# Kernel optimization log

Measured on AMD Instinct MI355X. Metric: run time of the kernel, lower is better.

## Reference

```python
import jax, jax.numpy as jnp
import numpy as np

LSTM = 256
NUM_CELLS = 5
BLOCKS = 6
TEMP = 5.0
TANH_C = 1.1


def setup_inputs() -> dict:
    key = jax.random.key(0)
    ks = jax.random.split(key, 8)
    s = 0.05  # small init so sigmoids/tanh stay in sane range
    return {
        "enc_w": jax.random.normal(ks[0], (5, LSTM), jnp.float32) * s,
        "w_ih": jax.random.normal(ks[1], (4 * LSTM, LSTM), jnp.float32) * s,
        "w_hh": jax.random.normal(ks[2], (4 * LSTM, LSTM), jnp.float32) * s,
        "b_ih": jax.random.normal(ks[3], (4 * LSTM,), jnp.float32) * s,
        "b_hh": jax.random.normal(ks[4], (4 * LSTM,), jnp.float32) * s,
        "w1": jax.random.normal(ks[5], (LSTM, LSTM), jnp.float32) * s,
        "w2": jax.random.normal(ks[6], (LSTM, LSTM), jnp.float32) * s,
        "v": jax.random.normal(ks[7], (LSTM,), jnp.float32) * s,
    }


def _lstm_cell(x, h, c, w_ih, w_hh, b_ih, b_hh):
    # torch.nn.LSTMCell gate order: i, f, g, o
    g = w_ih @ x + b_ih + w_hh @ h + b_hh  # [4*LSTM]
    i, f, gg, o = jnp.split(g, 4)
    i, f, o = jax.nn.sigmoid(i), jax.nn.sigmoid(f), jax.nn.sigmoid(o)
    c2 = f * c + i * jnp.tanh(gg)
    h2 = o * jnp.tanh(c2)
    return h2, c2


def _run_sampler(bkey, enc_w, w_ih, w_hh, b_ih, b_hh, w1, w2, v):
    zeros = jnp.zeros((LSTM,), jnp.float32)
    inputs = enc_w[0]  # encoder(0)
    anchors = []
    anchors_w1 = []
    prev_h = prev_c = zeros
    # first two layers: LSTM always fed zero state (faithful to source)
    for _ in range(2):
        prev_h, prev_c = _lstm_cell(inputs, zeros, zeros, w_ih, w_hh, b_ih, b_hh)
        anchors.append(zeros)
        anchors_w1.append(w1 @ prev_h)
    arc_seq, log_probs, entropies = [], [], []
    step = 0
    for layer_id in range(2, NUM_CELLS + 2):
        for _ in range(2):
            prev_h, prev_c = _lstm_cell(inputs, prev_h, prev_c, w_ih, w_hh, b_ih, b_hh)
            q = jnp.tanh(jnp.stack(anchors_w1[:layer_id]) + w2 @ prev_h)  # [layer_id, LSTM]
            logits = (q @ v) / TEMP  # [layer_id]
            logits = TANH_C * jnp.tanh(logits)
            skey = jax.random.fold_in(bkey, step); step += 1
            index = jax.random.categorical(skey, logits)
            lsm = jax.nn.log_softmax(logits)
            arc_seq.append(index)
            log_probs.append(-lsm[index])  # F.cross_entropy
            entropies.append(jax.lax.stop_gradient(-jnp.sum(lsm * jnp.exp(lsm))))
            inputs = jnp.stack(anchors[:layer_id])[index]
        prev_h, prev_c = _lstm_cell(inputs, prev_h, prev_c, w_ih, w_hh, b_ih, b_hh)
        anchors.append(prev_h)
        anchors_w1.append(w1 @ prev_h)
        inputs = enc_w[0]
    arc = jnp.stack(arc_seq)  # [2*NUM_CELLS] int
    return arc, sum(entropies), sum(log_probs), prev_c, prev_h


def reference(enc_w, w_ih, w_hh, b_ih, b_hh, w1, w2, v):
    key = jax.random.key(42)
    all_arc = []
    all_entropy = jnp.float32(0.0)
    all_log_prob = jnp.float32(0.0)
    c = h = None
    for b in range(BLOCKS):
        arc, ent, lp, c, h = _run_sampler(
            jax.random.fold_in(key, b), enc_w, w_ih, w_hh, b_ih, b_hh, w1, w2, v)
        all_arc.append(arc)
        all_entropy = all_entropy + ent
        all_log_prob = all_log_prob + lp
    return (jnp.stack(all_arc), all_log_prob, all_entropy, c[None, :], h[None, :])
```

## Files before the change

kernel.cpp:

```cpp
#include <hip/hip_runtime.h>
#include <stdint.h>


#define NBLK  6
#define PWG   8
#define THR   512
#define TINYF 1.17549435e-38f
#define HTAGB 0xC3B00000u
#define YTAGB 0xE1700000u
#define ITAGB 0xA5D00000u
#define DONE_MAGIC 0x444f4e45

typedef unsigned long long u64;
struct U2 { uint32_t x, y; };

#define W_DONE 0u
#define W_PART 64u
#define W_IDX  128u
#define W_HX   640u
#define W_YMB  25216u
#define W_NEED 126976u

#define S_READY 0u
#define S_DONE  192u
#define S_PART  224u
#define S_HP    320u
#define S_ACC   24896u
#define FXS     67108864.0f
#define READY_MAGIC 0x52454459

__device__ __forceinline__ U2 tf2x32(uint32_t k0, uint32_t k1,
                                     uint32_t c0, uint32_t c1) {
  uint32_t ks2 = k0 ^ k1 ^ 0x1BD11BDAu;
  uint32_t x0 = c0 + k0, x1 = c1 + k1;
#define TFR(r) { x0 += x1; x1 = (x1 << (r)) | (x1 >> (32 - (r))); x1 ^= x0; }
  TFR(13) TFR(15) TFR(26) TFR(6)   x0 += k1;  x1 += ks2 + 1u;
  TFR(17) TFR(29) TFR(16) TFR(24)  x0 += ks2; x1 += k0 + 2u;
  TFR(13) TFR(15) TFR(26) TFR(6)   x0 += k0;  x1 += k1 + 3u;
  TFR(17) TFR(29) TFR(16) TFR(24)  x0 += k1;  x1 += ks2 + 4u;
  TFR(13) TFR(15) TFR(26) TFR(6)   x0 += ks2; x1 += k0 + 5u;
#undef TFR
  U2 r; r.x = x0; r.y = x1; return r;
}

__device__ __forceinline__ float sigf(float x) {
  return 1.0f / (1.0f + expf(-x));
}
__device__ __forceinline__ void istore(int* p, int v) {
  __hip_atomic_store(p, v, __ATOMIC_RELAXED, __HIP_MEMORY_SCOPE_AGENT);
}
__device__ __forceinline__ int iload(const int* p) {
  return __hip_atomic_load(p, __ATOMIC_RELAXED, __HIP_MEMORY_SCOPE_AGENT);
}
__device__ __forceinline__ void hstore(u64* p, u64 v) {
  __hip_atomic_store(p, v, __ATOMIC_RELAXED, __HIP_MEMORY_SCOPE_AGENT);
}
__device__ __forceinline__ u64 hload(const u64* p) {
  return __hip_atomic_load(p, __ATOMIC_RELAXED, __HIP_MEMORY_SCOPE_AGENT);
}
__device__ __forceinline__ void fstore(float* p, float v) {
  __hip_atomic_store(p, v, __ATOMIC_RELAXED, __HIP_MEMORY_SCOPE_AGENT);
}
__device__ __forceinline__ float fload(const float* p) {
  return __hip_atomic_load(p, __ATOMIC_RELAXED, __HIP_MEMORY_SCOPE_AGENT);
}
__device__ __forceinline__ u64 pollw(const u64* p, uint32_t want) {
  u64 v;
  for (;;) {
    v = hload(p);
    if ((uint32_t)(v >> 32) == want) return v;
    __builtin_amdgcn_s_sleep(1);
  }
}

__global__ __launch_bounds__(THR, 2) void ctrl_v11(
    const float* __restrict__ enc_w,
    const float* __restrict__ wih,
    const float* __restrict__ whh,
    const float* __restrict__ b_ih,
    const float* __restrict__ b_hh,
    const float* __restrict__ w1,
    const float* __restrict__ w2,
    const float* __restrict__ vvec,
    unsigned char* __restrict__ ws,
    float* __restrict__ out) {

  const int b = blockIdx.x & 7;
  const int p = blockIdx.x >> 3;
  if (b >= NBLK) return;
  const int tid = threadIdx.x;

  int*   done = (int*)(ws + W_DONE);
  float* part = (float*)(ws + W_PART);
  u64*   idxw = (u64*)(ws + W_IDX);
  u64*   hx   = (u64*)(ws + W_HX);
  u64*   ymb  = (u64*)(ws + W_YMB);

  const int rl = tid & 127, s = tid >> 7;
  const int grow = (rl >> 5) * 256 + p * 32 + (rl & 31);
  const int k0 = s * 64;
  const int rr = tid & 255, ks = tid >> 8;
  const int cb = p * 32 + ks * 16;

  __shared__ __align__(16) float gateL[THR];
  __shared__ __align__(16) float hL[256], encL[256], vL[256];
  __shared__ __align__(16) float anchL[4][256];
  __shared__ __align__(16) float w2hS[256], aw1S[6][256];
  __shared__ __align__(16) float yL8[8][256];
  __shared__ float rowSumL[128], biasS[128], h2S[32];
  __shared__ float logitL[8];
  __shared__ int   selL;

  if (tid < 256) { encL[tid] = enc_w[tid]; vL[tid] = vvec[tid]; }
  if (tid < 128) {
    int r = (tid >> 5) * 256 + p * 32 + (tid & 31);
    biasS[tid] = b_ih[r] + b_hh[r];
  }

  float4 wihr[16], whhr[16];
  #pragma unroll
  for (int c = 0; c < 16; ++c) {
    wihr[c] = *(const float4*)(wih + grow * 256 + k0 + c * 4);
    whhr[c] = *(const float4*)(whh + grow * 256 + k0 + c * 4);
  }
  float w1c[16], w2c[16];
  #pragma unroll
  for (int j = 0; j < 16; ++j) {
    w1c[j] = w1[rr * 256 + cb + j];
    w2c[j] = w2[rr * 256 + cb + j];
  }
  __syncthreads();

  auto dotIH = [&](const float* x) {
    float a = 0.0f;
    #pragma unroll
    for (int c = 0; c < 16; ++c) {
      float4 xv = *(const float4*)(x + k0 + c * 4);
      float4 w = wihr[c];
      a += w.x * xv.x + w.y * xv.y + w.z * xv.z + w.w * xv.w;
    }
    return a;
  };
  auto dotHH = [&]() {
    float a = 0.0f;
    #pragma unroll
    for (int c = 0; c < 16; ++c) {
      float4 xv = *(const float4*)(hL + k0 + c * 4);
      float4 w = whhr[c];
      a += w.x * xv.x + w.y * xv.y + w.z * xv.z + w.w * xv.w;
    }
    return a;
  };

  const float encih = dotIH(encL);

  float cv = 0.0f;
  U2 bk = tf2x32(0u, 42u, 0u, (uint32_t)b);
  int k = 1, step = 0;
  float lpAcc = 0.0f, entAcc = 0.0f;

  auto cell = [&](float gacc, int mode, int aid, int cid) {
    gateL[tid] = gacc;
    __syncthreads();
    if (tid < 128) {
      float ssum = 0.0f;
      #pragma unroll
      for (int j = 0; j < 4; ++j) ssum += gateL[j * 128 + tid];
      rowSumL[tid] = ssum + biasS[tid];
    }
    __syncthreads();
    if (tid < 32) {
      float gi = rowSumL[tid],       gf = rowSumL[32 + tid];
      float gg2 = rowSumL[64 + tid], go = rowSumL[96 + tid];
      float c2 = sigf(gf) * cv + sigf(gi) * tanhf(gg2);
      float h2 = sigf(go) * tanhf(c2);
      cv = c2;
      h2S[tid] = h2;
      if (mode == 2) {
        if (b == NBLK - 1) { out[62 + p * 32 + tid] = cv; out[318 + p * 32 + tid] = h2; }
      } else {
        hstore(&hx[(k & 1) * 1536 + b * 256 + p * 32 + tid],
               ((u64)(HTAGB | (uint32_t)k) << 32) | (u64)__float_as_uint(h2));
      }
    }
    __syncthreads();
    if (mode == 2) return;

    {
      const float* wc = (mode == 1) ? w1c : w2c;
      float yp = 0.0f;
      #pragma unroll
      for (int j = 0; j < 16; ++j) yp += wc[j] * h2S[ks * 16 + j];
      gateL[tid] = yp;
    }
    __syncthreads();
    u64* mslot = ymb + (size_t)(k & 1) * 6192 + (b * 8 + p) * 129;
    if (tid < 128) {
      float ya = gateL[2 * tid]     + gateL[256 + 2 * tid];
      float yb = gateL[2 * tid + 1] + gateL[256 + 2 * tid + 1];
      hstore(mslot + tid,
             ((u64)__float_as_uint(yb) << 32) | (u64)__float_as_uint(ya));
    }
    __syncthreads();
    if (tid == 0)
      hstore(mslot + 128, ((u64)(YTAGB | (uint32_t)k) << 32) | 1u);

    if (tid < 256) {
      u64 v = pollw(&hx[(k & 1) * 1536 + b * 256 + tid], HTAGB | (uint32_t)k);
      float hv = __uint_as_float((uint32_t)v);
      hL[tid] = hv;
      if (mode == 1 && cid >= 0) anchL[cid][tid] = hv;
    }
    __syncthreads();

    if (p == 0) {
      if (tid < 8)
        pollw(ymb + (size_t)(k & 1) * 6192 + (b * 8 + tid) * 129 + 128,
              YTAGB | (uint32_t)k);
      __syncthreads();
      {
        int pw = tid >> 6, o = tid & 63;
        const u64* mb = ymb + (size_t)(k & 1) * 6192 + (b * 8 + pw) * 129;
        u64 wa = hload(mb + 2 * o), wb = hload(mb + 2 * o + 1);
        yL8[pw][4 * o + 0] = __uint_as_float((uint32_t)wa);
        yL8[pw][4 * o + 1] = __uint_as_float((uint32_t)(wa >> 32));
        yL8[pw][4 * o + 2] = __uint_as_float((uint32_t)wb);
        yL8[pw][4 * o + 3] = __uint_as_float((uint32_t)(wb >> 32));
      }
      __syncthreads();
      if (tid < 256) {
        float y = 0.0f;
        #pragma unroll
        for (int pw = 0; pw < 8; ++pw) y += yL8[pw][tid];
        if (mode == 1) aw1S[aid][tid] = y; else w2hS[tid] = y;
      }
      __syncthreads();
    }
    ++k;
  };

  auto resolve = [&](int L) -> int {
    if (p == 0) {
      int wv = tid >> 6, lane = tid & 63;
      if (wv < L) {
        float a = 0.0f;
        #pragma unroll
        for (int j = 0; j < 4; ++j) {
          int kk = j * 64 + lane;
          a += tanhf(aw1S[wv][kk] + w2hS[kk]) * vL[kk];
        }
        a += __shfl_down(a, 32);
        a += __shfl_down(a, 16);
        a += __shfl_down(a, 8);
        a += __shfl_down(a, 4);
        a += __shfl_down(a, 2);
        a += __shfl_down(a, 1);
        if (lane == 0) logitL[wv] = a;
      }
      __syncthreads();
      if (tid < 64) {
        float lg = 0.0f, sgum = -1e30f;
        if (tid < L) {
          lg = 1.1f * tanhf(logitL[tid] * 0.2f);
          U2 sk = tf2x32(bk.x, bk.y, 0u, (uint32_t)step);
          U2 r2 = tf2x32(sk.x, sk.y, 0u, (uint32_t)tid);
          uint32_t bits = r2.x ^ r2.y;
          float u = __uint_as_float((bits >> 9) | 0x3f800000u) - 1.0f;
          u = fmaxf(TINYF, u + TINYF);
          sgum = lg - logf(-logf(u));
        }
        int bi = 0;
        float best = __shfl(sgum, 0, 64);
        for (int j = 1; j < L; ++j) {
          float sj = __shfl(sgum, j, 64);
          if (sj > best) { best = sj; bi = j; }
        }
        float mx = __shfl(lg, 0, 64);
        for (int j = 1; j < L; ++j) mx = fmaxf(mx, __shfl(lg, j, 64));
        float se = 0.0f;
        for (int j = 0; j < L; ++j) se += expf(__shfl(lg, j, 64) - mx);
        float lse = logf(se);
        float lgbi = __shfl(lg, bi, 64);
        float es = 0.0f;
        for (int j = 0; j < L; ++j) {
          float l = __shfl(lg, j, 64) - mx - lse;
          es += l * expf(l);
        }
        if (tid == 0) {
          lpAcc += -(lgbi - mx - lse);
          entAcc += -es;
          selL = bi;
          out[b * 10 + step] = (float)bi;
          hstore(&idxw[b * 10 + step],
                 ((u64)(ITAGB | (uint32_t)step) << 32) | (u64)(uint32_t)bi);
        }
      }
      __syncthreads();
    } else {
      if (tid == 0) {
        u64 v = pollw(&idxw[b * 10 + step], ITAGB | (uint32_t)step);
        selL = (int)(uint32_t)v;
      }
      __syncthreads();
    }
    step++;
    return selL;
  };

  cell(encih, 1, 0, -1);
  if (p == 0) {
    if (tid < 256) aw1S[1][tid] = aw1S[0][tid];
    __syncthreads();
  }

  for (int L = 2; L <= 6; ++L) {
    { float hh = dotHH(); cell(encih + hh, 0, 0, -1); }
    {
      int s1; float hh;
      if (p == 0) { s1 = resolve(L); hh = dotHH(); }
      else        { hh = dotHH(); s1 = resolve(L); }
      float a = (s1 >= 2) ? dotIH(&anchL[s1 - 2][0]) : 0.0f;
      cell(a + hh, 0, 0, -1);
    }
    {
      int s2; float hh;
      if (p == 0) { s2 = resolve(L); hh = dotHH(); }
      else        { hh = dotHH(); s2 = resolve(L); }
      float a = (s2 >= 2) ? dotIH(&anchL[s2 - 2][0]) : 0.0f;
      if (L < 6) cell(a + hh, 1, L, L - 2);
      else       cell(a + hh, 2, 0, -1);
    }
  }

  if (p == 0 && tid == 0) {
    fstore(&part[2 * b], lpAcc);
    fstore(&part[2 * b + 1], entAcc);
    __builtin_amdgcn_s_waitcnt(0);
    istore(&done[b], DONE_MAGIC);
    if (b == NBLK - 1) {
      float lp = 0.0f, en = 0.0f;
      for (int j = 0; j < NBLK; ++j) {
        while (iload(&done[j]) != DONE_MAGIC) __builtin_amdgcn_s_sleep(1);
        lp += fload(&part[2 * j]);
        en += fload(&part[2 * j + 1]);
      }
      out[60] = lp;
      out[61] = en;
    }
  }
}

__global__ __launch_bounds__(1024) void ctrl_small(
    const float* __restrict__ enc_w,
    const float* __restrict__ wih,
    const float* __restrict__ whh,
    const float* __restrict__ b_ih,
    const float* __restrict__ b_hh,
    const float* __restrict__ w1,
    const float* __restrict__ w2,
    const float* __restrict__ vvec,
    unsigned char* __restrict__ ws,
    float* __restrict__ out) {

  const int b = blockIdx.x & 7;
  const int p = blockIdx.x >> 3;
  if (b >= NBLK) return;
  const int tid = threadIdx.x;

  int*   ready = (int*)(ws + S_READY);
  int*   done  = (int*)(ws + S_DONE);
  float* part  = (float*)(ws + S_PART);
  u64*   hp    = (u64*)(ws + S_HP);
  int*   acc   = (int*)(ws + S_ACC);

  const int rl = tid >> 3, s = tid & 7;
  const int g = rl >> 5, el = rl & 31;
  const int row = g * 256 + p * 32 + el;
  const int k0 = s * 32;
  const int rr = tid & 255, ks = tid >> 8;

  __shared__ __align__(16) float hL[256], encL[256], vL[256];
  __shared__ __align__(16) float anchL[4][256];
  __shared__ __align__(16) float partL[1024];
  __shared__ __align__(16) float w2hS[256], aw1S[6][256];
  __shared__ float rowSumL[128], biasS[128], h2S[32];
  __shared__ float logitL[8];
  __shared__ int   selL;

  if (tid < 256) { encL[tid] = enc_w[tid]; vL[tid] = vvec[tid]; }
  if (tid < 128) {
    int gg = tid >> 5, ee = tid & 31, r = gg * 256 + p * 32 + ee;
    biasS[tid] = b_ih[r] + b_hh[r];
  }

  float4 wihr[8], whhr[8];
  #pragma unroll
  for (int c = 0; c < 8; ++c) {
    int cc = (c + s) & 7;
    wihr[c] = *(const float4*)(wih + row * 256 + k0 + cc * 4);
    whhr[c] = *(const float4*)(whh + row * 256 + k0 + cc * 4);
  }
  float w1c[8], w2c[8];
  #pragma unroll
  for (int j = 0; j < 8; ++j) {
    w1c[j] = w1[rr * 256 + p * 32 + ks * 8 + j];
    w2c[j] = w2[rr * 256 + p * 32 + ks * 8 + j];
  }

  if (tid < 32) istore(&acc[1 * (NBLK * 256) + b * 256 + p * 32 + tid], 0);
  __syncthreads();
  if (tid == 0) istore(&ready[b * 8 + p], READY_MAGIC);
  if (tid < 8) {
    while (iload(&ready[b * 8 + tid]) != READY_MAGIC)
      __builtin_amdgcn_s_sleep(1);
  }
  __syncthreads();

  auto dotIH = [&](const float* x) {
    float a = 0.0f;
    #pragma unroll
    for (int c = 0; c < 8; ++c) {
      int cc = (c + s) & 7;
      float4 xv = *(const float4*)(x + k0 + cc * 4);
      float4 w = wihr[c];
      a += w.x * xv.x + w.y * xv.y + w.z * xv.z + w.w * xv.w;
    }
    return a;
  };
  auto dotHH = [&]() {
    float a = 0.0f;
    #pragma unroll
    for (int c = 0; c < 8; ++c) {
      int cc = (c + s) & 7;
      float4 xv = *(const float4*)(hL + k0 + cc * 4);
      float4 w = whhr[c];
      a += w.x * xv.x + w.y * xv.y + w.z * xv.z + w.w * xv.w;
    }
    return a;
  };

  const float encih = dotIH(encL);
  float cv = 0.0f;
  U2 bk = tf2x32(0u, 42u, 0u, (uint32_t)b);
  int k = 1, step = 0;
  float lpAcc = 0.0f, entAcc = 0.0f;

  auto cell = [&](float gacc, int mode, int aid, int cid) {
    partL[tid] = gacc;
    __syncthreads();
    if (tid < 128) {
      float ssum = 0.0f;
      #pragma unroll
      for (int j = 0; j < 8; ++j) ssum += partL[tid * 8 + j];
      rowSumL[tid] = ssum + biasS[tid];
    }
    __syncthreads();
    if (tid < 32) {
      float gi = rowSumL[tid],       gf = rowSumL[32 + tid];
      float gg2 = rowSumL[64 + tid], go = rowSumL[96 + tid];
      float c2 = sigf(gf) * cv + sigf(gi) * tanhf(gg2);
      float h2 = sigf(go) * tanhf(c2);
      cv = c2;
      h2S[tid] = h2;
      if (mode == 2 && b == NBLK - 1) {
        out[62 + p * 32 + tid] = cv;
        out[318 + p * 32 + tid] = h2;
      }
    }
    __syncthreads();
    if (mode == 2) return;
    {
      const float* wc = (mode == 1) ? w1c : w2c;
      float yp = 0.0f;
      #pragma unroll
      for (int j = 0; j < 8; ++j) yp += wc[j] * h2S[ks * 8 + j];
      atomicAdd(&acc[(k % 3) * (NBLK * 256) + b * 256 + rr],
                __float2int_rn(yp * FXS));
      if (tid < 32)
        istore(&acc[((k + 1) % 3) * (NBLK * 256) + b * 256 + p * 32 + tid], 0);
    }
    __syncthreads();
    if (tid < 32) {
      u64 pk = ((u64)(uint32_t)k << 32) | (u64)__float_as_uint(h2S[tid]);
      hstore(&hp[(k & 1) * (NBLK * 256) + b * 256 + p * 32 + tid], pk);
    }
    if (tid < 256) {
      u64 v;
      const u64* src = &hp[(k & 1) * (NBLK * 256) + b * 256 + tid];
      while ((int)(hload(src) >> 32) != k) __builtin_amdgcn_s_sleep(1);
      v = hload(src);
      float hv = __uint_as_float((uint32_t)v);
      hL[tid] = hv;
      if (mode == 1 && cid >= 0) anchL[cid][tid] = hv;
    }
    __syncthreads();
    if (tid < 256) {
      int iv = iload(&acc[(k % 3) * (NBLK * 256) + b * 256 + tid]);
      float f = (float)((double)iv * (1.0 / 67108864.0));
      if (mode == 1) aw1S[aid][tid] = f; else w2hS[tid] = f;
    }
    __syncthreads();
    ++k;
  };

  auto sample = [&](int L) -> int {
    int wv = tid >> 6, lane = tid & 63;
    if (wv < L) {
      float a = 0.0f;
      #pragma unroll
      for (int j = 0; j < 4; ++j) {
        int kk = lane * 4 + j;
        a += tanhf(aw1S[wv][kk] + w2hS[kk]) * vL[kk];
      }
      a += __shfl_down(a, 32);
      a += __shfl_down(a, 16);
      a += __shfl_down(a, 8);
      a += __shfl_down(a, 4);
      a += __shfl_down(a, 2);
      a += __shfl_down(a, 1);
      if (lane == 0) logitL[wv] = a;
    }
    __syncthreads();
    if (tid < 64) {
      float lg = 0.0f, sgum = -1e30f;
      if (tid < L) {
        lg = 1.1f * tanhf(logitL[tid] * 0.2f);
        U2 sk = tf2x32(bk.x, bk.y, 0u, (uint32_t)step);
        U2 r2 = tf2x32(sk.x, sk.y, 0u, (uint32_t)tid);
        uint32_t bits = r2.x ^ r2.y;
        float u = __uint_as_float((bits >> 9) | 0x3f800000u) - 1.0f;
        u = fmaxf(TINYF, u + TINYF);
        sgum = lg - logf(-logf(u));
      }
      int bi = 0;
      float best = __shfl(sgum, 0, 64);
      for (int j = 1; j < L; ++j) {
        float sj = __shfl(sgum, j, 64);
        if (sj > best) { best = sj; bi = j; }
      }
      float mx = __shfl(lg, 0, 64);
      for (int j = 1; j < L; ++j) mx = fmaxf(mx, __shfl(lg, j, 64));
      float se = 0.0f;
      for (int j = 0; j < L; ++j) se += expf(__shfl(lg, j, 64) - mx);
      float lse = logf(se);
      float lgbi = __shfl(lg, bi, 64);
      float es = 0.0f;
      for (int j = 0; j < L; ++j) {
        float l = __shfl(lg, j, 64) - mx - lse;
        es += l * expf(l);
      }
      if (tid == 0) {
        lpAcc += -(lgbi - mx - lse);
        entAcc += -es;
        selL = bi;
        if (p == 0) out[b * 10 + step] = (float)bi;
      }
    }
    __syncthreads();
    step++;
    return selL;
  };

  cell(encih, 1, 0, -1);
  if (tid < 256) aw1S[1][tid] = aw1S[0][tid];
  __syncthreads();
  for (int L = 2; L <= 6; ++L) {
    cell(encih + dotHH(), 0, 0, -1);
    int s1v = sample(L);
    {
      float a = (s1v >= 2) ? dotIH(&anchL[s1v - 2][0]) : 0.0f;
      cell(a + dotHH(), 0, 0, -1);
    }
    int s2v = sample(L);
    {
      float a = (s2v >= 2) ? dotIH(&anchL[s2v - 2][0]) : 0.0f;
      if (L < 6) cell(a + dotHH(), 1, L, L - 2);
      else       cell(a + dotHH(), 2, 0, -1);
    }
  }
  if (p == 0 && tid == 0) {
    fstore(&part[2 * b], lpAcc);
    fstore(&part[2 * b + 1], entAcc);
    __builtin_amdgcn_s_waitcnt(0);
    istore(&done[b], DONE_MAGIC);
    if (b == NBLK - 1) {
      float lp = 0.0f, en = 0.0f;
      for (int j = 0; j < NBLK; ++j) {
        while (iload(&done[j]) != DONE_MAGIC) __builtin_amdgcn_s_sleep(1);
        lp += fload(&part[2 * j]);
        en += fload(&part[2 * j + 1]);
      }
      out[60] = lp;
      out[61] = en;
    }
  }
}

extern "C" void kernel_launch(void* const* d_in, const int* in_sizes, int n_in,
                              void* d_out, int out_size, void* d_ws, size_t ws_size,
                              hipStream_t stream) {
  const float* enc = (const float*)d_in[0];
  const float* wih = (const float*)d_in[1];
  const float* whh = (const float*)d_in[2];
  const float* bih = (const float*)d_in[3];
  const float* bhh = (const float*)d_in[4];
  const float* w1  = (const float*)d_in[5];
  const float* w2  = (const float*)d_in[6];
  const float* v   = (const float*)d_in[7];
  unsigned char* ws = (unsigned char*)d_ws;
  float* out = (float*)d_out;

  if (ws_size >= W_NEED) {
    ctrl_v11<<<dim3(64), dim3(THR), 0, stream>>>(
        enc, wih, whh, bih, bhh, w1, w2, v, ws, out);
  } else {
    ctrl_small<<<dim3(64), dim3(1024), 0, stream>>>(
        enc, wih, whh, bih, bhh, w1, w2, v, ws, out);
  }
}
```

Measured before the change: 152.4 us.

## Replicate sampling on every workgroup and precompute anchor input projections

Every workgroup in a batch now reads the partial W1/W2 projections itself and runs the categorical sampling redundantly, with the same RNG. This removes the index broadcast from workgroup 0 and the extra poll round-trip that came with it. The input-weight dot product for each anchor is computed once, when the anchor is created, and kept in shared memory (aihS), so a later selection is just a lookup. W_ih is no longer held in registers, which lowers register pressure. The cost is duplicated reduction and sampling work in every workgroup, more global reads of the exchange buffers, and a hand-unrolled, fairly convoluted loop control flow.

```diff
diff --git a/kernel.cpp b/kernel.cpp
--- a/kernel.cpp
+++ b/kernel.cpp
@@ -8,7 +8,6 @@
 #define TINYF 1.17549435e-38f
 #define HTAGB 0xC3B00000u
 #define YTAGB 0xE1700000u
-#define ITAGB 0xA5D00000u
 #define DONE_MAGIC 0x444f4e45
 
 typedef unsigned long long u64;
@@ -16,10 +15,9 @@
 
 #define W_DONE 0u
 #define W_PART 64u
-#define W_IDX  128u
-#define W_HX   640u
-#define W_YMB  25216u
-#define W_NEED 126976u
+#define W_EX   512u
+#define EXBLK  161
+#define W_NEED 124160u
 
 #define S_READY 0u
 #define S_DONE  192u
@@ -73,7 +71,7 @@
   }
 }
 
-__global__ __launch_bounds__(THR, 2) void ctrl_v11(
+__global__ __launch_bounds__(THR, 2) void ctrl_v12(
     const float* __restrict__ enc_w,
     const float* __restrict__ wih,
     const float* __restrict__ whh,
@@ -92,9 +90,7 @@
 
   int*   done = (int*)(ws + W_DONE);
   float* part = (float*)(ws + W_PART);
-  u64*   idxw = (u64*)(ws + W_IDX);
-  u64*   hx   = (u64*)(ws + W_HX);
-  u64*   ymb  = (u64*)(ws + W_YMB);
+  u64*   ex   = (u64*)(ws + W_EX);
 
   const int rl = tid & 127, s = tid >> 7;
   const int grow = (rl >> 5) * 256 + p * 32 + (rl & 31);
@@ -104,12 +100,11 @@
 
   __shared__ __align__(16) float gateL[THR];
   __shared__ __align__(16) float hL[256], encL[256], vL[256];
-  __shared__ __align__(16) float anchL[4][256];
   __shared__ __align__(16) float w2hS[256], aw1S[6][256];
   __shared__ __align__(16) float yL8[8][256];
+  __shared__ __align__(16) float aihS[4][128];
   __shared__ float rowSumL[128], biasS[128], h2S[32];
   __shared__ float logitL[8];
-  __shared__ int   selL;
 
   if (tid < 256) { encL[tid] = enc_w[tid]; vL[tid] = vvec[tid]; }
   if (tid < 128) {
@@ -117,12 +112,10 @@
     biasS[tid] = b_ih[r] + b_hh[r];
   }
 
-  float4 wihr[16], whhr[16];
+  float4 whhr[16];
   #pragma unroll
-  for (int c = 0; c < 16; ++c) {
-    wihr[c] = *(const float4*)(wih + grow * 256 + k0 + c * 4);
+  for (int c = 0; c < 16; ++c)
     whhr[c] = *(const float4*)(whh + grow * 256 + k0 + c * 4);
-  }
   float w1c[16], w2c[16];
   #pragma unroll
   for (int j = 0; j < 16; ++j) {
@@ -131,16 +124,6 @@
   }
   __syncthreads();
 
-  auto dotIH = [&](const float* x) {
-    float a = 0.0f;
-    #pragma unroll
-    for (int c = 0; c < 16; ++c) {
-      float4 xv = *(const float4*)(x + k0 + c * 4);
-      float4 w = wihr[c];
-      a += w.x * xv.x + w.y * xv.y + w.z * xv.z + w.w * xv.w;
-    }
-    return a;
-  };
   auto dotHH = [&]() {
     float a = 0.0f;
     #pragma unroll
@@ -151,15 +134,26 @@
     }
     return a;
   };
-
-  const float encih = dotIH(encL);
+  auto dotIHg = [&](const float* x) {
+    const float4* wp = (const float4*)(wih + grow * 256 + k0);
+    float a = 0.0f;
+    #pragma unroll
+    for (int c = 0; c < 16; ++c) {
+      float4 w = wp[c];
+      float4 xv = *(const float4*)(x + k0 + c * 4);
+      a += w.x * xv.x + w.y * xv.y + w.z * xv.z + w.w * xv.w;
+    }
+    return a;
+  };
+
+  const float encih = dotIHg(encL);
 
   float cv = 0.0f;
   U2 bk = tf2x32(0u, 42u, 0u, (uint32_t)b);
-  int k = 1, step = 0;
+  int k = 1, kc = 0, step = 0;
   float lpAcc = 0.0f, entAcc = 0.0f;
 
-  auto cell = [&](float gacc, int mode, int aid, int cid) {
+  auto cell = [&](float gacc, bool isW1, bool last) {
     gateL[tid] = gacc;
     __syncthreads();
     if (tid < 128) {
@@ -169,6 +163,7 @@
       rowSumL[tid] = ssum + biasS[tid];
     }
     __syncthreads();
+    u64* blk = ex + (((size_t)(k & 1) * NBLK + b) * PWG + p) * EXBLK;
     if (tid < 32) {
       float gi = rowSumL[tid],       gf = rowSumL[32 + tid];
       float gg2 = rowSumL[64 + tid], go = rowSumL[96 + tid];
@@ -176,159 +171,205 @@
       float h2 = sigf(go) * tanhf(c2);
       cv = c2;
       h2S[tid] = h2;
-      if (mode == 2) {
+      if (last) {
         if (b == NBLK - 1) { out[62 + p * 32 + tid] = cv; out[318 + p * 32 + tid] = h2; }
       } else {
-        hstore(&hx[(k & 1) * 1536 + b * 256 + p * 32 + tid],
+        hstore(blk + 128 + tid,
                ((u64)(HTAGB | (uint32_t)k) << 32) | (u64)__float_as_uint(h2));
       }
     }
     __syncthreads();
-    if (mode == 2) return;
-
-    {
-      const float* wc = (mode == 1) ? w1c : w2c;
+    if (last) return;
+
+    {
+      const float* wc = isW1 ? w1c : w2c;
       float yp = 0.0f;
       #pragma unroll
       for (int j = 0; j < 16; ++j) yp += wc[j] * h2S[ks * 16 + j];
       gateL[tid] = yp;
     }
     __syncthreads();
-    u64* mslot = ymb + (size_t)(k & 1) * 6192 + (b * 8 + p) * 129;
     if (tid < 128) {
       float ya = gateL[2 * tid]     + gateL[256 + 2 * tid];
       float yb = gateL[2 * tid + 1] + gateL[256 + 2 * tid + 1];
-      hstore(mslot + tid,
+      hstore(blk + tid,
              ((u64)__float_as_uint(yb) << 32) | (u64)__float_as_uint(ya));
     }
     __syncthreads();
     if (tid == 0)
-      hstore(mslot + 128, ((u64)(YTAGB | (uint32_t)k) << 32) | 1u);
+      hstore(blk + 160, ((u64)(YTAGB | (uint32_t)k) << 32) | 1u);
 
     if (tid < 256) {
-      u64 v = pollw(&hx[(k & 1) * 1536 + b * 256 + tid], HTAGB | (uint32_t)k);
-      float hv = __uint_as_float((uint32_t)v);
-      hL[tid] = hv;
-      if (mode == 1 && cid >= 0) anchL[cid][tid] = hv;
-    }
-    __syncthreads();
-
-    if (p == 0) {
-      if (tid < 8)
-        pollw(ymb + (size_t)(k & 1) * 6192 + (b * 8 + tid) * 129 + 128,
-              YTAGB | (uint32_t)k);
-      __syncthreads();
-      {
-        int pw = tid >> 6, o = tid & 63;
-        const u64* mb = ymb + (size_t)(k & 1) * 6192 + (b * 8 + pw) * 129;
-        u64 wa = hload(mb + 2 * o), wb = hload(mb + 2 * o + 1);
-        yL8[pw][4 * o + 0] = __uint_as_float((uint32_t)wa);
-        yL8[pw][4 * o + 1] = __uint_as_float((uint32_t)(wa >> 32));
-        yL8[pw][4 * o + 2] = __uint_as_float((uint32_t)wb);
-        yL8[pw][4 * o + 3] = __uint_as_float((uint32_t)(wb >> 32));
-      }
-      __syncthreads();
-      if (tid < 256) {
-        float y = 0.0f;
-        #pragma unroll
-        for (int pw = 0; pw < 8; ++pw) y += yL8[pw][tid];
-        if (mode == 1) aw1S[aid][tid] = y; else w2hS[tid] = y;
-      }
-      __syncthreads();
-    }
+      const u64* base = ex + (((size_t)(k & 1) * NBLK + b) * PWG) * EXBLK;
+      u64 v = pollw(base + (size_t)(tid >> 5) * EXBLK + 128 + (tid & 31),
+                    HTAGB | (uint32_t)k);
+      hL[tid] = __uint_as_float((uint32_t)v);
+    }
+    __syncthreads();
+    kc = k;
     ++k;
   };
 
-  auto resolve = [&](int L) -> int {
-    if (p == 0) {
-      int wv = tid >> 6, lane = tid & 63;
-      if (wv < L) {
-        float a = 0.0f;
-        #pragma unroll
-        for (int j = 0; j < 4; ++j) {
-          int kk = j * 64 + lane;
-          a += tanhf(aw1S[wv][kk] + w2hS[kk]) * vL[kk];
-        }
-        a += __shfl_down(a, 32);
-        a += __shfl_down(a, 16);
-        a += __shfl_down(a, 8);
-        a += __shfl_down(a, 4);
-        a += __shfl_down(a, 2);
-        a += __shfl_down(a, 1);
-        if (lane == 0) logitL[wv] = a;
-      }
-      __syncthreads();
-      if (tid < 64) {
-        float lg = 0.0f, sgum = -1e30f;
-        if (tid < L) {
-          lg = 1.1f * tanhf(logitL[tid] * 0.2f);
-          U2 sk = tf2x32(bk.x, bk.y, 0u, (uint32_t)step);
-          U2 r2 = tf2x32(sk.x, sk.y, 0u, (uint32_t)tid);
-          uint32_t bits = r2.x ^ r2.y;
-          float u = __uint_as_float((bits >> 9) | 0x3f800000u) - 1.0f;
-          u = fmaxf(TINYF, u + TINYF);
-          sgum = lg - logf(-logf(u));
-        }
-        int bi = 0;
-        float best = __shfl(sgum, 0, 64);
-        for (int j = 1; j < L; ++j) {
-          float sj = __shfl(sgum, j, 64);
-          if (sj > best) { best = sj; bi = j; }
-        }
-        float mx = __shfl(lg, 0, 64);
-        for (int j = 1; j < L; ++j) mx = fmaxf(mx, __shfl(lg, j, 64));
+  auto finishY = [&](int aid, bool isW1) {
+    const u64* base = ex + (((size_t)(kc & 1) * NBLK + b) * PWG) * EXBLK;
+    if (tid < 8) pollw(base + (size_t)tid * EXBLK + 160, YTAGB | (uint32_t)kc);
+    __syncthreads();
+    {
+      int q = tid >> 6, w0 = (tid & 63) * 2;
+      const u64* mb = base + (size_t)q * EXBLK;
+      u64 wa = hload(mb + w0), wb = hload(mb + w0 + 1);
+      yL8[q][2 * w0 + 0] = __uint_as_float((uint32_t)wa);
+      yL8[q][2 * w0 + 1] = __uint_as_float((uint32_t)(wa >> 32));
+      yL8[q][2 * w0 + 2] = __uint_as_float((uint32_t)wb);
+      yL8[q][2 * w0 + 3] = __uint_as_float((uint32_t)(wb >> 32));
+    }
+    __syncthreads();
+    if (tid < 256) {
+      float y = 0.0f;
+      #pragma unroll
+      for (int q = 0; q < 8; ++q) y += yL8[q][tid];
+      if (isW1) aw1S[aid][tid] = y; else w2hS[tid] = y;
+    }
+    __syncthreads();
+  };
+
+  auto makeAih = [&](int cid) {
+    float a = dotIHg(hL);
+    gateL[tid] = a;
+    __syncthreads();
+    if (tid < 128) {
+      float ssum = 0.0f;
+      #pragma unroll
+      for (int j = 0; j < 4; ++j) ssum += gateL[j * 128 + tid];
+      aihS[cid][tid] = ssum;
+    }
+    __syncthreads();
+  };
+
+  auto sample = [&](int L) -> int {
+    int wv = tid >> 6, lane = tid & 63;
+    if (wv < L) {
+      float a = 0.0f;
+      #pragma unroll
+      for (int j = 0; j < 4; ++j) {
+        int kk = j * 64 + lane;
+        a += tanhf(aw1S[wv][kk] + w2hS[kk]) * vL[kk];
+      }
+      a += __shfl_down(a, 32);
+      a += __shfl_down(a, 16);
+      a += __shfl_down(a, 8);
+      a += __shfl_down(a, 4);
+      a += __shfl_down(a, 2);
+      a += __shfl_down(a, 1);
+      if (lane == 0) logitL[wv] = a;
+    }
+    __syncthreads();
+    int bi = 0;
+    {
+      float lg[6];
+      for (int i = 0; i < L; ++i) lg[i] = 1.1f * tanhf(logitL[i] * 0.2f);
+      U2 sk = tf2x32(bk.x, bk.y, 0u, (uint32_t)step);
+      float best = 0.0f;
+      for (int i = 0; i < L; ++i) {
+        U2 r2 = tf2x32(sk.x, sk.y, 0u, (uint32_t)i);
+        uint32_t bits = r2.x ^ r2.y;
+        float u = __uint_as_float((bits >> 9) | 0x3f800000u) - 1.0f;
+        u = fmaxf(TINYF, u + TINYF);
+        float sg = lg[i] - logf(-logf(u));
+        if (i == 0 || sg > best) { best = sg; bi = i; }
+      }
+      if (tid == 0) {
+        float mx = lg[0];
+        for (int i = 1; i < L; ++i) mx = fmaxf(mx, lg[i]);
         float se = 0.0f;
-        for (int j = 0; j < L; ++j) se += expf(__shfl(lg, j, 64) - mx);
+        for (int i = 0; i < L; ++i) se += expf(lg[i] - mx);
         float lse = logf(se);
-        float lgbi = __shfl(lg, bi, 64);
+        lpAcc += -(lg[bi] - mx - lse);
         float es = 0.0f;
-        for (int j = 0; j < L; ++j) {
-          float l = __shfl(lg, j, 64) - mx - lse;
+        for (int i = 0; i < L; ++i) {
+          float l = lg[i] - mx - lse;
           es += l * expf(l);
         }
-        if (tid == 0) {
-          lpAcc += -(lgbi - mx - lse);
-          entAcc += -es;
-          selL = bi;
-          out[b * 10 + step] = (float)bi;
-          hstore(&idxw[b * 10 + step],
-                 ((u64)(ITAGB | (uint32_t)step) << 32) | (u64)(uint32_t)bi);
+        entAcc += -es;
+        if (p == 0) out[b * 10 + step] = (float)bi;
+      }
+    }
+    __syncthreads();
+    step++;
+    return bi;
+  };
+
+  cell(encih, true, false);
+  finishY(0, true);
+  if (tid < 256) aw1S[1][tid] = aw1S[0][tid];
+  __syncthreads();
+
+  for (int L = 2; L <= 6; ++L) {
+    { float hh = dotHH(); cell(encih + hh, false, false); }
+    {
+      float hh = dotHH();
+      finishY(0, false);
+      int s1 = sample(L);
+      float a = (s1 >= 2 && s == 0) ? aihS[s1 - 2][rl] : 0.0f;
+      cell(a + hh, false, false);
+    }
+    {
+      float hh = dotHH();
+      finishY(0, false);
+      int s2 = sample(L);
+      float a = (s2 >= 2 && s == 0) ? aihS[s2 - 2][rl] : 0.0f;
+      if (L < 6) {
+        cell(a + hh, true, false);
+        float hh3 = dotHH();
+        finishY(L, true);
+        makeAih(L - 2);
+        cell(encih + hh3, false, false);
+        finishY(0, false);
+        int s1n = sample(L + 1);
+        float an = (s1n >= 2 && s == 0) ? aihS[s1n - 2][rl] : 0.0f;
+        float hhn = dotHH();
+        cell(an + hhn, false, false);
+        finishY(0, false);
+        int s2n = sample(L + 1);
+        float an2 = (s2n >= 2 && s == 0) ? aihS[s2n - 2][rl] : 0.0f;
+        float hhn2 = dotHH();
+        if (L + 1 < 6) cell(an2 + hhn2, true, false);
+        else           cell(an2 + hhn2, false, true);
+        if (L + 1 < 6) {
+          float hh4 = dotHH();
+          finishY(L + 1, true);
+          makeAih(L - 1);
+          gateL[tid] = hh4;
         }
-      }
-      __syncthreads();
-    } else {
-      if (tid == 0) {
-        u64 v = pollw(&idxw[b * 10 + step], ITAGB | (uint32_t)step);
-        selL = (int)(uint32_t)v;
-      }
-      __syncthreads();
-    }
-    step++;
-    return selL;
-  };
-
-  cell(encih, 1, 0, -1);
-  if (p == 0) {
-    if (tid < 256) aw1S[1][tid] = aw1S[0][tid];
-    __syncthreads();
-  }
-
-  for (int L = 2; L <= 6; ++L) {
-    { float hh = dotHH(); cell(encih + hh, 0, 0, -1); }
-    {
-      int s1; float hh;
-      if (p == 0) { s1 = resolve(L); hh = dotHH(); }
-      else        { hh = dotHH(); s1 = resolve(L); }
-      float a = (s1 >= 2) ? dotIH(&anchL[s1 - 2][0]) : 0.0f;
-      cell(a + hh, 0, 0, -1);
-    }
-    {
-      int s2; float hh;
-      if (p == 0) { s2 = resolve(L); hh = dotHH(); }
-      else        { hh = dotHH(); s2 = resolve(L); }
-      float a = (s2 >= 2) ? dotIH(&anchL[s2 - 2][0]) : 0.0f;
-      if (L < 6) cell(a + hh, 1, L, L - 2);
-      else       cell(a + hh, 2, 0, -1);
+        L = L + 1;
+        if (L < 6) {
+          float hh4 = gateL[tid];
+          __syncthreads();
+          cell(encih + hh4, false, false);
+          finishY(0, false);
+          int s1m = sample(L + 1);
+          float am = (s1m >= 2 && s == 0) ? aihS[s1m - 2][rl] : 0.0f;
+          float hhm = dotHH();
+          cell(am + hhm, false, false);
+          finishY(0, false);
+          int s2m = sample(L + 1);
+          float am2 = (s2m >= 2 && s == 0) ? aihS[s2m - 2][rl] : 0.0f;
+          float hhm2 = dotHH();
+          if (L + 1 < 6) {
+            cell(am2 + hhm2, true, false);
+            float hh5 = dotHH();
+            finishY(L + 1, true);
+            makeAih(L);
+            gateL[tid] = hh5;
+            __syncthreads();
+          } else {
+            cell(am2 + hhm2, false, true);
+          }
+          L = L + 1;
+        }
+      } else {
+        cell(a + hh, false, true);
+      }
     }
   }
 
@@ -611,7 +652,7 @@
   float* out = (float*)d_out;
 
   if (ws_size >= W_NEED) {
-    ctrl_v11<<<dim3(64), dim3(THR), 0, stream>>>(
+    ctrl_v12<<<dim3(64), dim3(THR), 0, stream>>>(
         enc, wih, whh, bih, bhh, w1, w2, v, ws, out);
   } else {
     ctrl_small<<<dim3(64), dim3(1024), 0, stream>>>(
```

New measurement: 173.6 us. 13.9% more time.

## Precompute anchor input projections and merge h/y exchange into tagged per-element slots

Applied to the files above, without the earlier changes.

Removes the register-resident w_ih copy and instead computes w_ih·anchor once per new anchor, caching the per-row partial results in shared memory so later cells just look them up. The h and y cross-workgroup exchanges are merged into one tagged per-element buffer per workgroup, so each y value carries its own tag and the separate flag word is gone. The gather of y into aw1/w2h is deferred to the point of use on the sampling workgroup, taking it off the cell critical path. It lowers register pressure and per-step dot products, at the cost of more polling words and a global reload of w_ih for each anchor projection.

```diff
diff --git a/kernel.cpp b/kernel.cpp
--- a/kernel.cpp
+++ b/kernel.cpp
@@ -15,11 +15,11 @@
 struct U2 { uint32_t x, y; };
 
 #define W_DONE 0u
-#define W_PART 64u
-#define W_IDX  128u
-#define W_HX   640u
-#define W_YMB  25216u
-#define W_NEED 126976u
+#define W_PART 32u
+#define W_IDX  96u
+#define W_EX   512u
+#define EXBLK  288
+#define W_NEED 221696u
 
 #define S_READY 0u
 #define S_DONE  192u
@@ -73,7 +73,7 @@
   }
 }
 
-__global__ __launch_bounds__(THR, 2) void ctrl_v11(
+__global__ __launch_bounds__(THR, 2) void ctrl_v13(
     const float* __restrict__ enc_w,
     const float* __restrict__ wih,
     const float* __restrict__ whh,
@@ -93,8 +93,7 @@
   int*   done = (int*)(ws + W_DONE);
   float* part = (float*)(ws + W_PART);
   u64*   idxw = (u64*)(ws + W_IDX);
-  u64*   hx   = (u64*)(ws + W_HX);
-  u64*   ymb  = (u64*)(ws + W_YMB);
+  u64*   ex   = (u64*)(ws + W_EX);
 
   const int rl = tid & 127, s = tid >> 7;
   const int grow = (rl >> 5) * 256 + p * 32 + (rl & 31);
@@ -104,9 +103,8 @@
 
   __shared__ __align__(16) float gateL[THR];
   __shared__ __align__(16) float hL[256], encL[256], vL[256];
-  __shared__ __align__(16) float anchL[4][256];
   __shared__ __align__(16) float w2hS[256], aw1S[6][256];
-  __shared__ __align__(16) float yL8[8][256];
+  __shared__ __align__(16) float aihS[4][128];
   __shared__ float rowSumL[128], biasS[128], h2S[32];
   __shared__ float logitL[8];
   __shared__ int   selL;
@@ -117,12 +115,10 @@
     biasS[tid] = b_ih[r] + b_hh[r];
   }
 
-  float4 wihr[16], whhr[16];
+  float4 whhr[16];
   #pragma unroll
-  for (int c = 0; c < 16; ++c) {
-    wihr[c] = *(const float4*)(wih + grow * 256 + k0 + c * 4);
+  for (int c = 0; c < 16; ++c)
     whhr[c] = *(const float4*)(whh + grow * 256 + k0 + c * 4);
-  }
   float w1c[16], w2c[16];
   #pragma unroll
   for (int j = 0; j < 16; ++j) {
@@ -131,16 +127,6 @@
   }
   __syncthreads();
 
-  auto dotIH = [&](const float* x) {
-    float a = 0.0f;
-    #pragma unroll
-    for (int c = 0; c < 16; ++c) {
-      float4 xv = *(const float4*)(x + k0 + c * 4);
-      float4 w = wihr[c];
-      a += w.x * xv.x + w.y * xv.y + w.z * xv.z + w.w * xv.w;
-    }
-    return a;
-  };
   auto dotHH = [&]() {
     float a = 0.0f;
     #pragma unroll
@@ -151,15 +137,26 @@
     }
     return a;
   };
-
-  const float encih = dotIH(encL);
+  auto dotIHg = [&](const float* x) {
+    const float4* wp = (const float4*)(wih + grow * 256 + k0);
+    float a = 0.0f;
+    #pragma unroll
+    for (int c = 0; c < 16; ++c) {
+      float4 w = wp[c];
+      float4 xv = *(const float4*)(x + k0 + c * 4);
+      a += w.x * xv.x + w.y * xv.y + w.z * xv.z + w.w * xv.w;
+    }
+    return a;
+  };
+
+  const float encihP = dotIHg(encL);
 
   float cv = 0.0f;
   U2 bk = tf2x32(0u, 42u, 0u, (uint32_t)b);
   int k = 1, step = 0;
   float lpAcc = 0.0f, entAcc = 0.0f;
 
-  auto cell = [&](float gacc, int mode, int aid, int cid) {
+  auto cell = [&](float gacc, bool yIsW1, bool last) {
     gateL[tid] = gacc;
     __syncthreads();
     if (tid < 128) {
@@ -169,6 +166,7 @@
       rowSumL[tid] = ssum + biasS[tid];
     }
     __syncthreads();
+    u64* blk = ex + (((size_t)(k & 1) * NBLK + b) * PWG + p) * EXBLK;
     if (tid < 32) {
       float gi = rowSumL[tid],       gf = rowSumL[32 + tid];
       float gg2 = rowSumL[64 + tid], go = rowSumL[96 + tid];
@@ -176,159 +174,167 @@
       float h2 = sigf(go) * tanhf(c2);
       cv = c2;
       h2S[tid] = h2;
-      if (mode == 2) {
+      if (last) {
         if (b == NBLK - 1) { out[62 + p * 32 + tid] = cv; out[318 + p * 32 + tid] = h2; }
       } else {
-        hstore(&hx[(k & 1) * 1536 + b * 256 + p * 32 + tid],
+        hstore(blk + 256 + tid,
                ((u64)(HTAGB | (uint32_t)k) << 32) | (u64)__float_as_uint(h2));
       }
     }
     __syncthreads();
-    if (mode == 2) return;
+    if (last) return;
 
     {
-      const float* wc = (mode == 1) ? w1c : w2c;
+      const float* wc = yIsW1 ? w1c : w2c;
       float yp = 0.0f;
       #pragma unroll
       for (int j = 0; j < 16; ++j) yp += wc[j] * h2S[ks * 16 + j];
       gateL[tid] = yp;
     }
     __syncthreads();
-    u64* mslot = ymb + (size_t)(k & 1) * 6192 + (b * 8 + p) * 129;
+    if (tid < 256) {
+      float yo = gateL[tid] + gateL[256 + tid];
+      hstore(blk + tid,
+             ((u64)(YTAGB | (uint32_t)k) << 32) | (u64)__float_as_uint(yo));
+    }
+    if (tid < 256) {
+      const u64* base = ex + (((size_t)(k & 1) * NBLK + b) * PWG) * EXBLK;
+      u64 v = pollw(base + (size_t)(tid >> 5) * EXBLK + 256 + (tid & 31),
+                    HTAGB | (uint32_t)k);
+      hL[tid] = __uint_as_float((uint32_t)v);
+    }
+    __syncthreads();
+    ++k;
+  };
+
+  auto gatherY = [&](float* dest) {
+    const uint32_t tg = YTAGB | (uint32_t)(k - 1);
+    const u64* base = ex + (((size_t)((k - 1) & 1) * NBLK + b) * PWG) * EXBLK;
+    float acc = 0.0f;
+    int e = tid & 255, q0 = tid >> 8;
+    #pragma unroll
+    for (int qq = 0; qq < 4; ++qq) {
+      int q = q0 + 2 * qq;
+      u64 v = pollw(base + (size_t)q * EXBLK + e, tg);
+      acc += __uint_as_float((uint32_t)v);
+    }
+    gateL[tid] = acc;
+    __syncthreads();
+    if (tid < 256) dest[tid] = gateL[tid] + gateL[256 + tid];
+    __syncthreads();
+  };
+
+  auto makeAih = [&](int cid) {
+    float a = dotIHg(hL);
+    gateL[tid] = a;
+    __syncthreads();
     if (tid < 128) {
-      float ya = gateL[2 * tid]     + gateL[256 + 2 * tid];
-      float yb = gateL[2 * tid + 1] + gateL[256 + 2 * tid + 1];
-      hstore(mslot + tid,
-             ((u64)__float_as_uint(yb) << 32) | (u64)__float_as_uint(ya));
-    }
-    __syncthreads();
-    if (tid == 0)
-      hstore(mslot + 128, ((u64)(YTAGB | (uint32_t)k) << 32) | 1u);
-
-    if (tid < 256) {
-      u64 v = pollw(&hx[(k & 1) * 1536 + b * 256 + tid], HTAGB | (uint32_t)k);
-      float hv = __uint_as_float((uint32_t)v);
-      hL[tid] = hv;
-      if (mode == 1 && cid >= 0) anchL[cid][tid] = hv;
-    }
-    __syncthreads();
-
-    if (p == 0) {
-      if (tid < 8)
-        pollw(ymb + (size_t)(k & 1) * 6192 + (b * 8 + tid) * 129 + 128,
-              YTAGB | (uint32_t)k);
-      __syncthreads();
-      {
-        int pw = tid >> 6, o = tid & 63;
-        const u64* mb = ymb + (size_t)(k & 1) * 6192 + (b * 8 + pw) * 129;
-        u64 wa = hload(mb + 2 * o), wb = hload(mb + 2 * o + 1);
-        yL8[pw][4 * o + 0] = __uint_as_float((uint32_t)wa);
-        yL8[pw][4 * o + 1] = __uint_as_float((uint32_t)(wa >> 32));
-        yL8[pw][4 * o + 2] = __uint_as_float((uint32_t)wb);
-        yL8[pw][4 * o + 3] = __uint_as_float((uint32_t)(wb >> 32));
-      }
-      __syncthreads();
-      if (tid < 256) {
-        float y = 0.0f;
-        #pragma unroll
-        for (int pw = 0; pw < 8; ++pw) y += yL8[pw][tid];
-        if (mode == 1) aw1S[aid][tid] = y; else w2hS[tid] = y;
-      }
-      __syncthreads();
-    }
-    ++k;
-  };
-
-  auto resolve = [&](int L) -> int {
-    if (p == 0) {
-      int wv = tid >> 6, lane = tid & 63;
-      if (wv < L) {
-        float a = 0.0f;
-        #pragma unroll
-        for (int j = 0; j < 4; ++j) {
-          int kk = j * 64 + lane;
-          a += tanhf(aw1S[wv][kk] + w2hS[kk]) * vL[kk];
-        }
-        a += __shfl_down(a, 32);
-        a += __shfl_down(a, 16);
-        a += __shfl_down(a, 8);
-        a += __shfl_down(a, 4);
-        a += __shfl_down(a, 2);
-        a += __shfl_down(a, 1);
-        if (lane == 0) logitL[wv] = a;
-      }
-      __syncthreads();
-      if (tid < 64) {
-        float lg = 0.0f, sgum = -1e30f;
-        if (tid < L) {
-          lg = 1.1f * tanhf(logitL[tid] * 0.2f);
-          U2 sk = tf2x32(bk.x, bk.y, 0u, (uint32_t)step);
-          U2 r2 = tf2x32(sk.x, sk.y, 0u, (uint32_t)tid);
-          uint32_t bits = r2.x ^ r2.y;
-          float u = __uint_as_float((bits >> 9) | 0x3f800000u) - 1.0f;
-          u = fmaxf(TINYF, u + TINYF);
-          sgum = lg - logf(-logf(u));
-        }
-        int bi = 0;
-        float best = __shfl(sgum, 0, 64);
-        for (int j = 1; j < L; ++j) {
-          float sj = __shfl(sgum, j, 64);
-          if (sj > best) { best = sj; bi = j; }
-        }
-        float mx = __shfl(lg, 0, 64);
-        for (int j = 1; j < L; ++j) mx = fmaxf(mx, __shfl(lg, j, 64));
-        float se = 0.0f;
-        for (int j = 0; j < L; ++j) se += expf(__shfl(lg, j, 64) - mx);
-        float lse = logf(se);
-        float lgbi = __shfl(lg, bi, 64);
-        float es = 0.0f;
-        for (int j = 0; j < L; ++j) {
-          float l = __shfl(lg, j, 64) - mx - lse;
-          es += l * expf(l);
-        }
-        if (tid == 0) {
-          lpAcc += -(lgbi - mx - lse);
-          entAcc += -es;
-          selL = bi;
-          out[b * 10 + step] = (float)bi;
-          hstore(&idxw[b * 10 + step],
-                 ((u64)(ITAGB | (uint32_t)step) << 32) | (u64)(uint32_t)bi);
-        }
-      }
-      __syncthreads();
-    } else {
+      float ssum = 0.0f;
+      #pragma unroll
+      for (int j = 0; j < 4; ++j) ssum += gateL[j * 128 + tid];
+      aihS[cid][tid] = ssum;
+    }
+    __syncthreads();
+  };
+
+  auto sampleStep = [&](int L) -> int {
+    int wv = tid >> 6, lane = tid & 63;
+    if (wv < L) {
+      float a = 0.0f;
+      #pragma unroll
+      for (int j = 0; j < 4; ++j) {
+        int kk = j * 64 + lane;
+        a += tanhf(aw1S[wv][kk] + w2hS[kk]) * vL[kk];
+      }
+      a += __shfl_down(a, 32);
+      a += __shfl_down(a, 16);
+      a += __shfl_down(a, 8);
+      a += __shfl_down(a, 4);
+      a += __shfl_down(a, 2);
+      a += __shfl_down(a, 1);
+      if (lane == 0) logitL[wv] = a;
+    }
+    __syncthreads();
+    if (tid < 64) {
+      float lg = 0.0f, sgum = -1e30f;
+      if (tid < L) {
+        lg = 1.1f * tanhf(logitL[tid] * 0.2f);
+        U2 sk = tf2x32(bk.x, bk.y, 0u, (uint32_t)step);
+        U2 r2 = tf2x32(sk.x, sk.y, 0u, (uint32_t)tid);
+        uint32_t bits = r2.x ^ r2.y;
+        float u = __uint_as_float((bits >> 9) | 0x3f800000u) - 1.0f;
+        u = fmaxf(TINYF, u + TINYF);
+        sgum = lg - logf(-logf(u));
+      }
+      int bi = 0;
+      float best = __shfl(sgum, 0, 64);
+      for (int j = 1; j < L; ++j) {
+        float sj = __shfl(sgum, j, 64);
+        if (sj > best) { best = sj; bi = j; }
+      }
+      float mx = __shfl(lg, 0, 64);
+      for (int j = 1; j < L; ++j) mx = fmaxf(mx, __shfl(lg, j, 64));
+      float se = 0.0f;
+      for (int j = 0; j < L; ++j) se += expf(__shfl(lg, j, 64) - mx);
+      float lse = logf(se);
+      float lgbi = __shfl(lg, bi, 64);
+      float es = 0.0f;
+      for (int j = 0; j < L; ++j) {
+        float l = __shfl(lg, j, 64) - mx - lse;
+        es += l * expf(l);
+      }
       if (tid == 0) {
-        u64 v = pollw(&idxw[b * 10 + step], ITAGB | (uint32_t)step);
-        selL = (int)(uint32_t)v;
-      }
-      __syncthreads();
-    }
+        lpAcc += -(lgbi - mx - lse);
+        entAcc += -es;
+        selL = bi;
+        out[b * 10 + step] = (float)bi;
+        hstore(&idxw[b],
+               ((u64)(ITAGB | (uint32_t)step) << 32) | (u64)(uint32_t)bi);
+      }
+    }
+    __syncthreads();
     step++;
     return selL;
   };
 
-  cell(encih, 1, 0, -1);
+  auto pollIdx = [&]() -> int {
+    if (tid == 0) {
+      u64 v = pollw(&idxw[b], ITAGB | (uint32_t)step);
+      selL = (int)(uint32_t)v;
+    }
+    __syncthreads();
+    step++;
+    return selL;
+  };
+
+  cell(encihP, true, false);
   if (p == 0) {
+    gatherY(&aw1S[0][0]);
     if (tid < 256) aw1S[1][tid] = aw1S[0][tid];
     __syncthreads();
   }
 
   for (int L = 2; L <= 6; ++L) {
-    { float hh = dotHH(); cell(encih + hh, 0, 0, -1); }
+    { float hh = dotHH(); cell(encihP + hh, false, false); }
     {
       int s1; float hh;
-      if (p == 0) { s1 = resolve(L); hh = dotHH(); }
-      else        { hh = dotHH(); s1 = resolve(L); }
-      float a = (s1 >= 2) ? dotIH(&anchL[s1 - 2][0]) : 0.0f;
-      cell(a + hh, 0, 0, -1);
+      if (p == 0) { gatherY(w2hS); s1 = sampleStep(L); hh = dotHH(); }
+      else        { hh = dotHH(); s1 = pollIdx(); }
+      float aacc = (s1 >= 2 && s == 0) ? aihS[s1 - 2][rl] : 0.0f;
+      cell(aacc + hh, false, false);
     }
     {
       int s2; float hh;
-      if (p == 0) { s2 = resolve(L); hh = dotHH(); }
-      else        { hh = dotHH(); s2 = resolve(L); }
-      float a = (s2 >= 2) ? dotIH(&anchL[s2 - 2][0]) : 0.0f;
-      if (L < 6) cell(a + hh, 1, L, L - 2);
-      else       cell(a + hh, 2, 0, -1);
+      if (p == 0) { gatherY(w2hS); s2 = sampleStep(L); hh = dotHH(); }
+      else        { hh = dotHH(); s2 = pollIdx(); }
+      float aacc = (s2 >= 2 && s == 0) ? aihS[s2 - 2][rl] : 0.0f;
+      if (L < 6) {
+        cell(aacc + hh, true, false);
+        if (p == 0) gatherY(&aw1S[L][0]);
+        makeAih(L - 2);
+      } else {
+        cell(aacc + hh, false, true);
+      }
     }
   }
 
@@ -611,7 +617,7 @@
   float* out = (float*)d_out;
 
   if (ws_size >= W_NEED) {
-    ctrl_v11<<<dim3(64), dim3(THR), 0, stream>>>(
+    ctrl_v13<<<dim3(64), dim3(THR), 0, stream>>>(
         enc, wih, whh, bih, bhh, w1, w2, v, ws, out);
   } else {
     ctrl_small<<<dim3(64), dim3(1024), 0, stream>>>(
```

Measured after the change: 162.8 us. 6.9% more time.
